# Kernel tuning notes

Hardware: AMD Instinct MI355X
Metric: run time of the kernel (lower is better)

The kernel has to match this reference:

```python
import jax, jax.numpy as jnp
import numpy as np

B, T, V, E, H, NC = 256, 512, 128, 128, 256, 10000


def setup_inputs() -> dict:
    key = jax.random.key(0)
    ks = jax.random.split(key, 10)
    return {
        "dec_input_batch": jax.random.randint(ks[0], (B, T), 0, V),
        "dec_input_lengths": jax.random.randint(ks[1], (B,), 1, T + 1),
        "max_prob_clusters": jax.random.randint(ks[2], (B,), 0, NC),
        "char_embeddings": jax.random.normal(ks[3], (V, E), dtype=jnp.float32) * 0.1,
        "cluster_embeddings": jax.random.normal(ks[4], (NC, H), dtype=jnp.float32) * 0.1,
        "W0": jax.random.normal(ks[5], (E + H + H, 4 * H), dtype=jnp.float32) * 0.05,
        "b0": jnp.zeros((4 * H,), jnp.float32),
        "W1": jax.random.normal(ks[6], (H + H, 4 * H), dtype=jnp.float32) * 0.05,
        "b1": jnp.zeros((4 * H,), jnp.float32),
        "decoderW": jax.random.normal(ks[7], (H, V), dtype=jnp.float32) * (1.0 / (H + V)),
        "decoderB": jnp.zeros((V,), jnp.float32),
    }


def _lstm_step(c, h, x, W, b):
    # TF BasicLSTMCell: gates order i, j, f, o; forget_bias = 1.0
    z = jnp.concatenate([x, h], axis=-1) @ W + b
    i, j, f, o = jnp.split(z, 4, axis=-1)
    c2 = c * jax.nn.sigmoid(f + 1.0) + jax.nn.sigmoid(i) * jnp.tanh(j)
    h2 = jnp.tanh(c2) * jax.nn.sigmoid(o)
    return c2, h2


def reference(dec_input_batch, dec_input_lengths, max_prob_clusters,
              char_embeddings, cluster_embeddings, W0, b0, W1, b1,
              decoderW, decoderB):
    Bb, Tt = dec_input_batch.shape
    Hh = decoderW.shape[0]
    x = char_embeddings[dec_input_batch]                       # [B,T,E]
    clus = cluster_embeddings[max_prob_clusters]               # [B,H]
    clus_bt = jnp.broadcast_to(clus[:, None, :], (Bb, Tt, clus.shape[-1]))
    x = jnp.concatenate([x, clus_bt], axis=-1)                 # [B,T,E+H]
    xs = jnp.transpose(x, (1, 0, 2))                           # [T,B,E+H]
    # dynamic_rnn sequence_length semantics: past length -> zero output, state copied through
    mask = (jnp.arange(Tt)[:, None] < dec_input_lengths[None, :])[..., None]  # [T,B,1]
    zeros = jnp.zeros((Bb, Hh), x.dtype)

    def step(carry, inp):
        c0, h0, c1, h1 = carry
        xt, m = inp
        c0n, h0n = _lstm_step(c0, h0, xt, W0, b0)
        c1n, h1n = _lstm_step(c1, h1, h0n, W1, b1)
        c0 = jnp.where(m, c0n, c0); h0 = jnp.where(m, h0n, h0)
        c1 = jnp.where(m, c1n, c1); h1 = jnp.where(m, h1n, h1)
        out = jnp.where(m, h1n, jnp.zeros_like(h1n))
        return (c0, h0, c1, h1), out

    _, outs = jax.lax.scan(step, (zeros, zeros, zeros, zeros), (xs, mask))
    outs = jnp.transpose(outs, (1, 0, 2))                      # [B,T,H]
    raw_scores = outs @ decoderW + decoderB                    # [B,T,V]
    return raw_scores
```

## Files before the change

kernel.cpp:

```cpp
#include <hip/hip_runtime.h>

#define B_ 256
#define T_ 512
#define V_ 128
#define E_ 128
#define H_ 256
#define FH 1024

#define GROUPS 32
#define RPG 8
#define CWG 16
#define NWG (GROUPS*CWG)

#define HTG 2048
#define GST (GROUPS*HTG)

typedef float f4 __attribute__((ext_vector_type(4)));
typedef unsigned long long ull;

#define OFF_HT0  0
#define OFF_HT1  (OFF_HT0 + 2*GST)
#define OFF_BAR  (OFF_HT1 + 2*GST)
#define BARSZ    (GROUPS*1024)
#define OFF_TP   (OFF_BAR + BARSZ)
#define OFF_CP   (OFF_TP + V_*FH)
#define OFF_WP0  (OFF_CP + B_*FH)
#define OFF_WP1  (OFF_WP0 + CWG*64*64*4)
#define OFF_DWT  (OFF_WP1 + CWG*128*64*4)
#define OFF_B1   (OFF_DWT + V_*H_)
#define OFF_PERM (OFF_B1 + FH)

__device__ __forceinline__ int gcol(int c, int col) {
  int u = col >> 2, g = col & 3;
  return g*256 + c*16 + u;
}

__device__ __forceinline__ float sigm(float x){ return 1.f/(1.f+__expf(-x)); }
__device__ __forceinline__ float tanh_(float x){ return 1.f - 2.f/(1.f+__expf(2.f*x)); }


__global__ void prep_pack(const float* __restrict__ W0, const float* __restrict__ W1,
                          const float* __restrict__ dW, const float* __restrict__ b1,
                          float* __restrict__ ws) {
  float* wp0 = ws + OFF_WP0; float* wp1 = ws + OFF_WP1;
  float* dwT = ws + OFF_DWT; float* b1p = ws + OFF_B1;
  const int N0 = CWG*64*64*4;
  const int N1 = CWG*128*64*4;
  const int N2 = V_*H_;
  const int N3 = FH;
  const int total = N0+N1+N2+N3;
  for (int i = blockIdx.x*blockDim.x + threadIdx.x; i < total; i += gridDim.x*blockDim.x) {
    if (i < N0) {
      int cc = i >> 14; int rem = i & 16383;
      int kb = rem >> 8; int ln = (rem >> 2) & 63; int j = i & 3;
      int k = kb*4 + j;
      wp0[i] = W0[(E_+H_+k)*FH + gcol(cc, ln)];
    } else if (i < N0+N1) {
      int idx = i - N0;
      int cc = idx >> 15; int rem = idx & 32767;
      int kb = rem >> 8; int ln = (rem >> 2) & 63; int j = idx & 3;
      int k2 = kb*4 + j;
      wp1[idx] = W1[k2*FH + gcol(cc, ln)];
    } else if (i < N0+N1+N2) {
      int l = i - N0 - N1;
      int v = l >> 8, k = l & 255;
      dwT[l] = dW[k*V_ + v];
    } else {
      int cc2 = i - N0 - N1 - N2;
      b1p[cc2] = b1[gcol(cc2>>6, cc2&63)];
    }
  }
}

__global__ void prep_tok(const float* __restrict__ cemb, const float* __restrict__ W0,
                         float* __restrict__ ws) {
  __shared__ float ce[E_];
  float* TP = ws + OFF_TP;
  int v = blockIdx.x >> 2, q = blockIdx.x & 3;
  int tid = threadIdx.x;
  if (tid < E_) ce[tid] = cemb[v*E_ + tid];
  __syncthreads();
  int ccol = q*256 + tid;
  int G = gcol(ccol>>6, ccol&63);
  float acc = 0.f;
  for (int e = 0; e < E_; ++e) acc = fmaf(ce[e], W0[e*FH + G], acc);
  TP[v*FH + ccol] = acc;
}

__global__ void prep_clus(const int* __restrict__ clus, const float* __restrict__ clemb,
                          const float* __restrict__ W0, const float* __restrict__ b0,
                          float* __restrict__ ws) {
  __shared__ float ce[H_];
  float* CP = ws + OFF_CP;
  int b = blockIdx.x >> 2, q = blockIdx.x & 3;
  int tid = threadIdx.x;
  int cl = clus[b];
  ce[tid] = clemb[(long long)cl*H_ + tid];
  __syncthreads();
  int ccol = q*256 + tid;
  int G = gcol(ccol>>6, ccol&63);
  float acc = b0[G];
  for (int e = 0; e < H_; ++e) acc = fmaf(ce[e], W0[(E_+e)*FH + G], acc);
  CP[b*FH + ccol] = acc;
}

__global__ void prep_sort(const int* __restrict__ lens, float* __restrict__ ws) {
  __shared__ int sl[B_];
  int* perm = (int*)(ws + OFF_PERM);
  const int i = threadIdx.x;
  sl[i] = lens[i];
  __syncthreads();
  const int li = sl[i];
  int rank = 0;
  for (int j = 0; j < B_; ++j) {
    const int lj = sl[j];
    rank += (lj > li) || (lj == li && j < i);
  }
  perm[rank] = i;
}


__device__ __forceinline__ void st64(float* p, float a, float b) {
  float2 t; t.x = a; t.y = b;
  __hip_atomic_store((ull*)p, __builtin_bit_cast(ull, t),
                     __ATOMIC_RELAXED, __HIP_MEMORY_SCOPE_AGENT);
}

__device__ __forceinline__ void st64_sc0(float* p, float a, float b) {
  float2 t; t.x = a; t.y = b;
  ull v = __builtin_bit_cast(ull, t);
  asm volatile("global_store_dwordx2 %0, %1, off sc0" :: "v"(p), "v"(v) : "memory");
}

__device__ __forceinline__ ull ld64(const void* p) {
  return __hip_atomic_load((const ull*)p, __ATOMIC_RELAXED, __HIP_MEMORY_SCOPE_AGENT);
}

__device__ __forceinline__ unsigned ld32_sc0(const unsigned* p) {
  unsigned v;
  asm volatile("global_load_dword %0, %1, off sc0\n\t"
               "s_waitcnt vmcnt(0)"
               : "=v"(v) : "v"(p) : "memory");
  return v;
}

__device__ __forceinline__ void flag_set(unsigned* p, unsigned v) {
  asm volatile("s_waitcnt vmcnt(0)" ::: "memory");
  __hip_atomic_store(p, v, __ATOMIC_RELAXED, __HIP_MEMORY_SCOPE_AGENT);
}
__device__ __forceinline__ void flag_set_sc0(unsigned* p, unsigned v) {
  asm volatile("s_waitcnt vmcnt(0)" ::: "memory");
  asm volatile("global_store_dword %0, %1, off sc0" :: "v"(p), "v"(v) : "memory");
}

__device__ __forceinline__ void spinAB(const unsigned* fgrp, int lane, unsigned tgt) {
  const unsigned* p = fgrp + (lane & 15)*32 + ((lane >> 5) << 4);
  unsigned v = __hip_atomic_load(p, __ATOMIC_RELAXED, __HIP_MEMORY_SCOPE_AGENT);
  while (!__all((int)(v >= tgt))) {
    __builtin_amdgcn_s_sleep(4);
    v = __hip_atomic_load(p, __ATOMIC_RELAXED, __HIP_MEMORY_SCOPE_AGENT);
  }
}
__device__ __forceinline__ void spinAB_fast(const unsigned* fgrp, int lane, unsigned tgt) {
  const unsigned* p = fgrp + (lane & 15)*32 + ((lane >> 5) << 4);
  unsigned v = ld32_sc0(p);
  int it = 0;
  while (!__all((int)(v >= tgt))) {
    __builtin_amdgcn_s_sleep(2);
    ++it;
    v = (it & 7) ? ld32_sc0(p)
                 : __hip_atomic_load(p, __ATOMIC_RELAXED, __HIP_MEMORY_SCOPE_AGENT);
  }
}

__device__ __forceinline__ void spinB(const unsigned* fgrp, int lane, unsigned tgt) {
  const unsigned* p = fgrp + (lane & 15)*32 + 16;
  unsigned v = __hip_atomic_load(p, __ATOMIC_RELAXED, __HIP_MEMORY_SCOPE_AGENT);
  while (!__all((int)(v >= tgt))) {
    __builtin_amdgcn_s_sleep(4);
    v = __hip_atomic_load(p, __ATOMIC_RELAXED, __HIP_MEMORY_SCOPE_AGENT);
  }
}

__device__ __forceinline__ void lstm_gate(const f4 z, float& cc, float& hh, const bool upd) {
  float ci = sigm(z.x);
  float cj = tanh_(z.y);
  float cf = sigm(z.z + 1.f);
  float co = sigm(z.w);
  float cn = fmaf(cc, cf, ci*cj);
  float hn = tanh_(cn)*co;
  if (upd) { cc = cn; hh = hn; }
}


__global__ __launch_bounds__(256, 2) void lstm_persist(
    const int* __restrict__ toks, const int* __restrict__ lens,
    const float* __restrict__ decB, float* __restrict__ ws, float* __restrict__ out)
{
  const int blk  = blockIdx.x;
  const int xcd  = blk & 7;
  const int j    = blk >> 3;
  const int grp  = (xcd << 2) | ((j & 1) << 1) | (j >> 5);
  const int c    = (j >> 1) & 15;
  const int tid  = threadIdx.x;
  const int lane = tid & 63;
  const int wv   = tid >> 6;
  const int cof  = c*64;

  const int sgrp  = ((grp & 3) << 3) | (grp >> 2);
  const int rbase = sgrp*RPG;
  const int* perm = (const int*)(ws + OFF_PERM);

  float* ht0 = ws + OFF_HT0;
  float* ht1 = ws + OFF_HT1;
  unsigned* fgrp = (unsigned*)(ws + OFF_BAR) + grp*1024;
  const float* TP   = ws + OFF_TP;
  const float* CP   = ws + OFF_CP;
  const float* wp0c = ws + OFF_WP0 + c*(64*64*4);
  const float* wp1c = ws + OFF_WP1 + c*(128*64*4);
  const float* dwT  = ws + OFF_DWT;
  const float* b1p  = ws + OFF_B1;

  __shared__ __align__(16) float h0s[2048];
  __shared__ __align__(16) float h1s[2048];
  __shared__ __align__(16) float za[4][8][64];
  __shared__ __align__(16) float zb[4][8][64];
  __shared__ float ldsW[8][260];
  __shared__ float pred[2][4][64];
  __shared__ unsigned fastSh;

  for (int i = tid; i < 8*H_; i += 256)
    ldsW[i>>8][i&255] = dwT[(c*8 + (i>>8))*H_ + (i&255)];

  unsigned xcc;
  asm volatile("s_getreg_b32 %0, hwreg(HW_REG_XCC_ID)" : "=s"(xcc));
  if (tid == 0)
    __hip_atomic_store(fgrp + 512 + c, xcc + 1u, __ATOMIC_RELAXED, __HIP_MEMORY_SCOPE_AGENT);
  if (wv == 0) {
    const unsigned* p = fgrp + 512 + (lane & 15);
    unsigned v = __hip_atomic_load(p, __ATOMIC_RELAXED, __HIP_MEMORY_SCOPE_AGENT);
    while (!__all((int)(v != 0u))) {
      __builtin_amdgcn_s_sleep(8);
      v = __hip_atomic_load(p, __ATOMIC_RELAXED, __HIP_MEMORY_SCOPE_AGENT);
    }
    const bool same = __all((int)(v == xcc + 1u));
    if (lane == 0) fastSh = same ? 1u : 0u;
  }

  int Lg = lens[perm[rbase + (lane & 7)]];
  Lg = max(Lg, __shfl_xor(Lg, 1));
  Lg = max(Lg, __shfl_xor(Lg, 2));
  Lg = max(Lg, __shfl_xor(Lg, 4));

  const int gu = lane & 15, q = lane >> 4;
  const int rowA = perm[rbase + q], rowB = perm[rbase + q + 4];
  const int lenA = lens[rowA], lenB = lens[rowB];
  const int* tokApt = toks + rowA*T_;
  const int* tokBpt = toks + rowB*T_;
  const f4 cpA = *(const f4*)(CP + rowA*FH + cof + gu*4);
  const f4 cpB = *(const f4*)(CP + rowB*FH + cof + gu*4);
  const f4 b1v = *(const f4*)(b1p + cof + gu*4);
  const int puboff = grp*HTG + (c*16 + gu)*8 + q*2;
  float c0A = 0.f, h0A = 0.f, c0B = 0.f, h0B = 0.f;
  float c1A = 0.f, h1A = 0.f, c1B = 0.f, h1B = 0.f;

  const int pm = lane >> 3, pv = lane & 7;
  const int prm = (pm < 4) ? pm*2 : (pm-4)*2 + 1;
  const int prow = perm[rbase + pm];
  const int plen = lens[prow];
  const float decb = decB[c*8 + pv];
  float* outp = out + (size_t)prow*T_*V_ + c*8 + pv;

  __syncthreads();
  const bool fast = (fastSh != 0u);

  if (wv == 0) {
    f4 zAv = *(const f4*)(TP + tokApt[0]*FH + cof + gu*4) + cpA;
    f4 zBv = *(const f4*)(TP + tokBpt[0]*FH + cof + gu*4) + cpB;
    lstm_gate(zAv, c0A, h0A, 0 < lenA);
    lstm_gate(zBv, c0B, h0B, 0 < lenB);
    if (fast) st64_sc0(ht0 + puboff, h0A, h0B);
    else      st64(ht0 + puboff, h0A, h0B);
    if (lane == 0) {
      if (fast) flag_set_sc0(fgrp + c*32, 1u);
      else      flag_set(fgrp + c*32, 1u);
    }
  } else if (wv == 1) {
    if (lane == 0) {
      if (fast) flag_set_sc0(fgrp + c*32 + 16, 1u);
      else      flag_set(fgrp + c*32 + 16, 1u);
    }
  }

  for (int t = 0; t < Lg; ++t) {
    const int buf = t & 1;

    f4 tpA = {0,0,0,0}, tpB = {0,0,0,0};
    if (wv == 0 && t + 1 < Lg) {
      tpA = *(const f4*)(TP + tokApt[t+1]*FH + cof + gu*4);
      tpB = *(const f4*)(TP + tokBpt[t+1]*FH + cof + gu*4);
    }

    if (fast) spinAB_fast(fgrp, lane, (unsigned)(t + 1));
    else      spinAB(fgrp, lane, (unsigned)(t + 1));
    __atomic_signal_fence(__ATOMIC_SEQ_CST);

    {
      const float* s0 = ht0 + buf*GST + grp*HTG + wv*512 + lane*8;
      const float* s1 = ht1 + buf*GST + grp*HTG + wv*512 + lane*8;
      ull a0, a1, a2, a3, c0, c1, c2, c3;
      if (fast) {
        asm volatile(
          "global_load_dwordx2 %0, %8, off sc0\n\t"
          "global_load_dwordx2 %1, %8, off offset:8 sc0\n\t"
          "global_load_dwordx2 %2, %8, off offset:16 sc0\n\t"
          "global_load_dwordx2 %3, %8, off offset:24 sc0\n\t"
          "global_load_dwordx2 %4, %9, off sc0\n\t"
          "global_load_dwordx2 %5, %9, off offset:8 sc0\n\t"
          "global_load_dwordx2 %6, %9, off offset:16 sc0\n\t"
          "global_load_dwordx2 %7, %9, off offset:24 sc0\n\t"
          "s_waitcnt vmcnt(0)"
          : "=&v"(a0), "=&v"(a1), "=&v"(a2), "=&v"(a3),
            "=&v"(c0), "=&v"(c1), "=&v"(c2), "=&v"(c3)
          : "v"(s0), "v"(s1)
          : "memory");
      } else {
        a0 = ld64(s0);   a1 = ld64(s0+2); a2 = ld64(s0+4); a3 = ld64(s0+6);
        c0 = ld64(s1);   c1 = ld64(s1+2); c2 = ld64(s1+4); c3 = ld64(s1+6);
      }
      float* d0 = h0s + wv*512 + lane*8;
      float* d1 = h1s + wv*512 + lane*8;
      *(ull*)(d0)   = a0; *(ull*)(d0+2) = a1; *(ull*)(d0+4) = a2; *(ull*)(d0+6) = a3;
      *(ull*)(d1)   = c0; *(ull*)(d1+2) = c1; *(ull*)(d1+4) = c2; *(ull*)(d1+6) = c3;
    }

    f4 A0l = {0,0,0,0}, A0h = {0,0,0,0}, A1l = {0,0,0,0}, A1h = {0,0,0,0};
    #pragma unroll 2
    for (int b = 0; b < 16; ++b) {
      const int kb = wv*16 + b;
      const f4 w0 = *(const f4*)(wp0c + kb*256 + lane*4);
      const f4 wl = *(const f4*)(wp1c + kb*256 + lane*4);
      const f4 wu = *(const f4*)(wp1c + (64 + kb)*256 + lane*4);
      #pragma unroll
      for (int jj = 0; jj < 4; ++jj) {
        const int k = kb*4 + jj;
        const float* hb0 = h0s + k*8;
        const float* hb1 = h1s + k*8;
        const f4 h0lo = *(const f4*)(hb0);
        const f4 h0hi = *(const f4*)(hb0 + 4);
        const f4 h1lo = *(const f4*)(hb1);
        const f4 h1hi = *(const f4*)(hb1 + 4);
        const float w0j = w0[jj], wlj = wl[jj], wuj = wu[jj];
        A0l += w0j * h0lo;  A0h += w0j * h0hi;
        A1l += wlj * h0lo + wuj * h1lo;
        A1h += wlj * h0hi + wuj * h1hi;
      }
    }

    float pacc = 0.f;
    {
      const int kq = wv*64;
      #pragma unroll 4
      for (int k2 = 0; k2 < 64; k2 += 4) {
        const f4 w4 = *(const f4*)&ldsW[pv][kq + k2];
        pacc = fmaf(h1s[(kq+k2  )*8 + prm], w4.x, pacc);
        pacc = fmaf(h1s[(kq+k2+1)*8 + prm], w4.y, pacc);
        pacc = fmaf(h1s[(kq+k2+2)*8 + prm], w4.z, pacc);
        pacc = fmaf(h1s[(kq+k2+3)*8 + prm], w4.w, pacc);
      }
    }

    #pragma unroll
    for (int r = 0; r < 4; ++r) {
      za[wv][r][lane]     = A0l[r];
      za[wv][4 + r][lane] = A0h[r];
      zb[wv][r][lane]     = A1l[r];
      zb[wv][4 + r][lane] = A1h[r];
    }
    pred[buf][wv][lane] = pacc;
    __syncthreads();

    if (wv == 0) {
      if (t + 1 < Lg) {
        f4 zA = *(const f4*)&za[0][q*2][gu*4];
        zA += *(const f4*)&za[1][q*2][gu*4];
        zA += *(const f4*)&za[2][q*2][gu*4];
        zA += *(const f4*)&za[3][q*2][gu*4];
        f4 zB = *(const f4*)&za[0][q*2+1][gu*4];
        zB += *(const f4*)&za[1][q*2+1][gu*4];
        zB += *(const f4*)&za[2][q*2+1][gu*4];
        zB += *(const f4*)&za[3][q*2+1][gu*4];
        zA += tpA + cpA;
        zB += tpB + cpB;
        lstm_gate(zA, c0A, h0A, (t+1) < lenA);
        lstm_gate(zB, c0B, h0B, (t+1) < lenB);
        float* pb = ht0 + (buf^1)*GST + puboff;
        if (fast) st64_sc0(pb, h0A, h0B);
        else      st64(pb, h0A, h0B);
        if (lane == 0) {
          if (fast) flag_set_sc0(fgrp + c*32, (unsigned)(t + 2));
          else      flag_set(fgrp + c*32, (unsigned)(t + 2));
        }
      }
    } else if (wv == 1) {
      f4 zA = *(const f4*)&zb[0][q*2][gu*4];
      zA += *(const f4*)&zb[1][q*2][gu*4];
      zA += *(const f4*)&zb[2][q*2][gu*4];
      zA += *(const f4*)&zb[3][q*2][gu*4];
      f4 zB = *(const f4*)&zb[0][q*2+1][gu*4];
      zB += *(const f4*)&zb[1][q*2+1][gu*4];
      zB += *(const f4*)&zb[2][q*2+1][gu*4];
      zB += *(const f4*)&zb[3][q*2+1][gu*4];
      zA += b1v;
      zB += b1v;
      lstm_gate(zA, c1A, h1A, t < lenA);
      lstm_gate(zB, c1B, h1B, t < lenB);
      float* pb = ht1 + (buf^1)*GST + puboff;
      if (fast) st64_sc0(pb, h1A, h1B);
      else      st64(pb, h1A, h1B);
      if (lane == 0) {
        if (fast) flag_set_sc0(fgrp + c*32 + 16, (unsigned)(t + 2));
        else      flag_set(fgrp + c*32 + 16, (unsigned)(t + 2));
      }
    } else if (wv == 2) {
      if (t > 0) {
        float tot = pred[buf][0][lane] + pred[buf][1][lane]
                  + pred[buf][2][lane] + pred[buf][3][lane] + decb;
        if (t - 1 < plen) outp[(size_t)(t-1)*V_] = tot;
      }
    }
  }

  spinB(fgrp, lane, (unsigned)(Lg + 1));
  __atomic_signal_fence(__ATOMIC_SEQ_CST);
  {
    const float* s1 = ht1 + (size_t)(Lg & 1)*GST + grp*HTG + wv*512 + lane*8;
    ull b0 = ld64(s1),   b1 = ld64(s1+2);
    ull b2 = ld64(s1+4), b3 = ld64(s1+6);
    float* d1 = h1s + wv*512 + lane*8;
    *(ull*)(d1)   = b0; *(ull*)(d1+2) = b1;
    *(ull*)(d1+4) = b2; *(ull*)(d1+6) = b3;
  }
  {
    float pacc = 0.f;
    const int kq = wv*64;
    #pragma unroll 4
    for (int k2 = 0; k2 < 64; k2 += 4) {
      const f4 w4 = *(const f4*)&ldsW[pv][kq + k2];
      pacc = fmaf(h1s[(kq+k2  )*8 + prm], w4.x, pacc);
      pacc = fmaf(h1s[(kq+k2+1)*8 + prm], w4.y, pacc);
      pacc = fmaf(h1s[(kq+k2+2)*8 + prm], w4.z, pacc);
      pacc = fmaf(h1s[(kq+k2+3)*8 + prm], w4.w, pacc);
    }
    pred[Lg & 1][wv][lane] = pacc;
  }
  __syncthreads();
  if (wv == 2) {
    float tot = pred[Lg & 1][0][lane] + pred[Lg & 1][1][lane]
              + pred[Lg & 1][2][lane] + pred[Lg & 1][3][lane] + decb;
    if (Lg - 1 < plen) outp[(size_t)(Lg-1)*V_] = tot;
  }
}


extern "C" void kernel_launch(void* const* d_in, const int* in_sizes, int n_in,
                              void* d_out, int out_size, void* d_ws, size_t ws_size,
                              hipStream_t stream) {
  const int*   toks  = (const int*)d_in[0];
  const int*   lens  = (const int*)d_in[1];
  const int*   clus  = (const int*)d_in[2];
  const float* cemb  = (const float*)d_in[3];
  const float* clemb = (const float*)d_in[4];
  const float* W0    = (const float*)d_in[5];
  const float* b0    = (const float*)d_in[6];
  const float* W1    = (const float*)d_in[7];
  const float* b1    = (const float*)d_in[8];
  const float* dW    = (const float*)d_in[9];
  const float* decB  = (const float*)d_in[10];
  float* out = (float*)d_out;
  float* ws  = (float*)d_ws;

  hipMemsetAsync(out, 0, (size_t)B_*T_*V_*sizeof(float), stream);
  hipMemsetAsync(ws, 0, (size_t)(OFF_BAR + BARSZ)*sizeof(float), stream);

  prep_pack<<<1024, 256, 0, stream>>>(W0, W1, dW, b1, ws);
  prep_tok <<<V_*4, 256, 0, stream>>>(cemb, W0, ws);
  prep_clus<<<B_*4, 256, 0, stream>>>(clus, clemb, W0, b0, ws);
  prep_sort<<<1, 256, 0, stream>>>(lens, ws);
  lstm_persist<<<NWG, 256, 0, stream>>>(toks, lens, decB, ws, out);
}
```

Baseline: 4.574 ms.

## Merge two column chunks per 512-thread workgroup in persistent LSTM kernel

The persistent kernel now runs 256 workgroups of 512 threads instead of 512 workgroups of 256. Each workgroup handles two 64-column gate chunks, one per four-wave half, and both halves share the staged h0/h1 buffers and the reduction arrays in LDS. The aim is to cut redundant global hidden-state loads and the number of workgroups polling the flags. The decoder weight tile is no longer staged in LDS and is read directly from global memory each step, which may add per-step load latency. Both halves also write the same LDS h buffers redundantly.

```diff
diff --git a/kernel.cpp b/kernel.cpp
--- a/kernel.cpp
+++ b/kernel.cpp
@@ -10,7 +10,8 @@
 #define GROUPS 32
 #define RPG 8
 #define CWG 16
-#define NWG (GROUPS*CWG)
+#define WGPG 8
+#define NWG (GROUPS*WGPG)
 
 #define HTG 2048
 #define GST (GROUPS*HTG)
@@ -193,21 +194,25 @@
 }
 
 
-__global__ __launch_bounds__(256, 2) void lstm_persist(
+__global__ __launch_bounds__(512, 2) void lstm_persist(
     const int* __restrict__ toks, const int* __restrict__ lens,
     const float* __restrict__ decB, float* __restrict__ ws, float* __restrict__ out)
 {
   const int blk  = blockIdx.x;
   const int xcd  = blk & 7;
   const int j    = blk >> 3;
-  const int grp  = (xcd << 2) | ((j & 1) << 1) | (j >> 5);
-  const int c    = (j >> 1) & 15;
+  const int cc   = j & 7;
+  const int loc  = j >> 3;
+  const int grp  = (xcd << 2) | loc;
   const int tid  = threadIdx.x;
   const int lane = tid & 63;
   const int wv   = tid >> 6;
-  const int cof  = c*64;
-
-  const int sgrp  = ((grp & 3) << 3) | (grp >> 2);
+  const int ch   = wv >> 2;
+  const int kwin = wv & 3;
+  const int ca   = cc*2 + ch;
+  const int cof  = ca*64;
+
+  const int sgrp  = (loc << 3) | xcd;
   const int rbase = sgrp*RPG;
   const int* perm = (const int*)(ws + OFF_PERM);
 
@@ -216,28 +221,24 @@
   unsigned* fgrp = (unsigned*)(ws + OFF_BAR) + grp*1024;
   const float* TP   = ws + OFF_TP;
   const float* CP   = ws + OFF_CP;
-  const float* wp0c = ws + OFF_WP0 + c*(64*64*4);
-  const float* wp1c = ws + OFF_WP1 + c*(128*64*4);
+  const float* wp0c = ws + OFF_WP0 + ca*(64*64*4);
+  const float* wp1c = ws + OFF_WP1 + ca*(128*64*4);
   const float* dwT  = ws + OFF_DWT;
   const float* b1p  = ws + OFF_B1;
 
-  __shared__ __align__(16) float h0s[2048];
-  __shared__ __align__(16) float h1s[2048];
-  __shared__ __align__(16) float za[4][8][64];
-  __shared__ __align__(16) float zb[4][8][64];
-  __shared__ float ldsW[8][260];
-  __shared__ float pred[2][4][64];
+  __shared__ __align__(16) float h0s[4*512];
+  __shared__ __align__(16) float h1s[4*512];
+  __shared__ __align__(16) float za[4][8][128];
+  __shared__ __align__(16) float zb[4][8][128];
+  __shared__ float pred[2][4][2][64];
   __shared__ unsigned fastSh;
-
-  for (int i = tid; i < 8*H_; i += 256)
-    ldsW[i>>8][i&255] = dwT[(c*8 + (i>>8))*H_ + (i&255)];
 
   unsigned xcc;
   asm volatile("s_getreg_b32 %0, hwreg(HW_REG_XCC_ID)" : "=s"(xcc));
   if (tid == 0)
-    __hip_atomic_store(fgrp + 512 + c, xcc + 1u, __ATOMIC_RELAXED, __HIP_MEMORY_SCOPE_AGENT);
+    __hip_atomic_store(fgrp + 512 + cc, xcc + 1u, __ATOMIC_RELAXED, __HIP_MEMORY_SCOPE_AGENT);
   if (wv == 0) {
-    const unsigned* p = fgrp + 512 + (lane & 15);
+    const unsigned* p = fgrp + 512 + (lane & 7);
     unsigned v = __hip_atomic_load(p, __ATOMIC_RELAXED, __HIP_MEMORY_SCOPE_AGENT);
     while (!__all((int)(v != 0u))) {
       __builtin_amdgcn_s_sleep(8);
@@ -260,7 +261,7 @@
   const f4 cpA = *(const f4*)(CP + rowA*FH + cof + gu*4);
   const f4 cpB = *(const f4*)(CP + rowB*FH + cof + gu*4);
   const f4 b1v = *(const f4*)(b1p + cof + gu*4);
-  const int puboff = grp*HTG + (c*16 + gu)*8 + q*2;
+  const int puboff = grp*HTG + (ca*16 + gu)*8 + q*2;
   float c0A = 0.f, h0A = 0.f, c0B = 0.f, h0B = 0.f;
   float c1A = 0.f, h1A = 0.f, c1B = 0.f, h1B = 0.f;
 
@@ -268,13 +269,14 @@
   const int prm = (pm < 4) ? pm*2 : (pm-4)*2 + 1;
   const int prow = perm[rbase + pm];
   const int plen = lens[prow];
-  const float decb = decB[c*8 + pv];
-  float* outp = out + (size_t)prow*T_*V_ + c*8 + pv;
+  const float decb = decB[ca*8 + pv];
+  float* outp = out + (size_t)prow*T_*V_ + ca*8 + pv;
+  const float* dwRow = dwT + (ca*8 + pv)*H_;
 
   __syncthreads();
   const bool fast = (fastSh != 0u);
 
-  if (wv == 0) {
+  if ((wv & 3) == 0) {
     f4 zAv = *(const f4*)(TP + tokApt[0]*FH + cof + gu*4) + cpA;
     f4 zBv = *(const f4*)(TP + tokBpt[0]*FH + cof + gu*4) + cpB;
     lstm_gate(zAv, c0A, h0A, 0 < lenA);
@@ -282,13 +284,13 @@
     if (fast) st64_sc0(ht0 + puboff, h0A, h0B);
     else      st64(ht0 + puboff, h0A, h0B);
     if (lane == 0) {
-      if (fast) flag_set_sc0(fgrp + c*32, 1u);
-      else      flag_set(fgrp + c*32, 1u);
-    }
-  } else if (wv == 1) {
+      if (fast) flag_set_sc0(fgrp + ca*32, 1u);
+      else      flag_set(fgrp + ca*32, 1u);
+    }
+  } else if ((wv & 3) == 1) {
     if (lane == 0) {
-      if (fast) flag_set_sc0(fgrp + c*32 + 16, 1u);
-      else      flag_set(fgrp + c*32 + 16, 1u);
+      if (fast) flag_set_sc0(fgrp + ca*32 + 16, 1u);
+      else      flag_set(fgrp + ca*32 + 16, 1u);
     }
   }
 
@@ -296,7 +298,7 @@
     const int buf = t & 1;
 
     f4 tpA = {0,0,0,0}, tpB = {0,0,0,0};
-    if (wv == 0 && t + 1 < Lg) {
+    if ((wv & 3) == 0 && t + 1 < Lg) {
       tpA = *(const f4*)(TP + tokApt[t+1]*FH + cof + gu*4);
       tpB = *(const f4*)(TP + tokBpt[t+1]*FH + cof + gu*4);
     }
@@ -306,8 +308,8 @@
     __atomic_signal_fence(__ATOMIC_SEQ_CST);
 
     {
-      const float* s0 = ht0 + buf*GST + grp*HTG + wv*512 + lane*8;
-      const float* s1 = ht1 + buf*GST + grp*HTG + wv*512 + lane*8;
+      const float* s0 = ht0 + buf*GST + grp*HTG + kwin*512 + lane*8;
+      const float* s1 = ht1 + buf*GST + grp*HTG + kwin*512 + lane*8;
       ull a0, a1, a2, a3, c0, c1, c2, c3;
       if (fast) {
         asm volatile(
@@ -328,8 +330,8 @@
         a0 = ld64(s0);   a1 = ld64(s0+2); a2 = ld64(s0+4); a3 = ld64(s0+6);
         c0 = ld64(s1);   c1 = ld64(s1+2); c2 = ld64(s1+4); c3 = ld64(s1+6);
       }
-      float* d0 = h0s + wv*512 + lane*8;
-      float* d1 = h1s + wv*512 + lane*8;
+      float* d0 = h0s + kwin*512 + lane*8;
+      float* d1 = h1s + kwin*512 + lane*8;
       *(ull*)(d0)   = a0; *(ull*)(d0+2) = a1; *(ull*)(d0+4) = a2; *(ull*)(d0+6) = a3;
       *(ull*)(d1)   = c0; *(ull*)(d1+2) = c1; *(ull*)(d1+4) = c2; *(ull*)(d1+6) = c3;
     }
@@ -337,15 +339,15 @@
     f4 A0l = {0,0,0,0}, A0h = {0,0,0,0}, A1l = {0,0,0,0}, A1h = {0,0,0,0};
     #pragma unroll 2
     for (int b = 0; b < 16; ++b) {
-      const int kb = wv*16 + b;
+      const int kb = kwin*16 + b;
       const f4 w0 = *(const f4*)(wp0c + kb*256 + lane*4);
       const f4 wl = *(const f4*)(wp1c + kb*256 + lane*4);
       const f4 wu = *(const f4*)(wp1c + (64 + kb)*256 + lane*4);
       #pragma unroll
       for (int jj = 0; jj < 4; ++jj) {
-        const int k = kb*4 + jj;
-        const float* hb0 = h0s + k*8;
-        const float* hb1 = h1s + k*8;
+        const int kl = b*4 + jj;
+        const float* hb0 = h0s + kwin*512 + kl*8;
+        const float* hb1 = h1s + kwin*512 + kl*8;
         const f4 h0lo = *(const f4*)(hb0);
         const f4 h0hi = *(const f4*)(hb0 + 4);
         const f4 h1lo = *(const f4*)(hb1);
@@ -359,37 +361,38 @@
 
     float pacc = 0.f;
     {
-      const int kq = wv*64;
+      const float* wrow = dwRow + kwin*64;
       #pragma unroll 4
       for (int k2 = 0; k2 < 64; k2 += 4) {
-        const f4 w4 = *(const f4*)&ldsW[pv][kq + k2];
-        pacc = fmaf(h1s[(kq+k2  )*8 + prm], w4.x, pacc);
-        pacc = fmaf(h1s[(kq+k2+1)*8 + prm], w4.y, pacc);
-        pacc = fmaf(h1s[(kq+k2+2)*8 + prm], w4.z, pacc);
-        pacc = fmaf(h1s[(kq+k2+3)*8 + prm], w4.w, pacc);
+        const f4 w4 = *(const f4*)(wrow + k2);
+        pacc = fmaf(h1s[kwin*512 + (k2  )*8 + prm], w4.x, pacc);
+        pacc = fmaf(h1s[kwin*512 + (k2+1)*8 + prm], w4.y, pacc);
+        pacc = fmaf(h1s[kwin*512 + (k2+2)*8 + prm], w4.z, pacc);
+        pacc = fmaf(h1s[kwin*512 + (k2+3)*8 + prm], w4.w, pacc);
       }
     }
 
     #pragma unroll
     for (int r = 0; r < 4; ++r) {
-      za[wv][r][lane]     = A0l[r];
-      za[wv][4 + r][lane] = A0h[r];
-      zb[wv][r][lane]     = A1l[r];
-      zb[wv][4 + r][lane] = A1h[r];
-    }
-    pred[buf][wv][lane] = pacc;
+      za[kwin][r][ch*64 + lane]     = A0l[r];
+      za[kwin][4 + r][ch*64 + lane] = A0h[r];
+      zb[kwin][r][ch*64 + lane]     = A1l[r];
+      zb[kwin][4 + r][ch*64 + lane] = A1h[r];
+    }
+    pred[buf][kwin][ch][lane] = pacc;
     __syncthreads();
 
-    if (wv == 0) {
+    const int cb = ch*64;
+    if ((wv & 3) == 0) {
       if (t + 1 < Lg) {
-        f4 zA = *(const f4*)&za[0][q*2][gu*4];
-        zA += *(const f4*)&za[1][q*2][gu*4];
-        zA += *(const f4*)&za[2][q*2][gu*4];
-        zA += *(const f4*)&za[3][q*2][gu*4];
-        f4 zB = *(const f4*)&za[0][q*2+1][gu*4];
-        zB += *(const f4*)&za[1][q*2+1][gu*4];
-        zB += *(const f4*)&za[2][q*2+1][gu*4];
-        zB += *(const f4*)&za[3][q*2+1][gu*4];
+        f4 zA = *(const f4*)&za[0][q*2][cb + gu*4];
+        zA += *(const f4*)&za[1][q*2][cb + gu*4];
+        zA += *(const f4*)&za[2][q*2][cb + gu*4];
+        zA += *(const f4*)&za[3][q*2][cb + gu*4];
+        f4 zB = *(const f4*)&za[0][q*2+1][cb + gu*4];
+        zB += *(const f4*)&za[1][q*2+1][cb + gu*4];
+        zB += *(const f4*)&za[2][q*2+1][cb + gu*4];
+        zB += *(const f4*)&za[3][q*2+1][cb + gu*4];
         zA += tpA + cpA;
         zB += tpB + cpB;
         lstm_gate(zA, c0A, h0A, (t+1) < lenA);
@@ -398,19 +401,19 @@
         if (fast) st64_sc0(pb, h0A, h0B);
         else      st64(pb, h0A, h0B);
         if (lane == 0) {
-          if (fast) flag_set_sc0(fgrp + c*32, (unsigned)(t + 2));
-          else      flag_set(fgrp + c*32, (unsigned)(t + 2));
+          if (fast) flag_set_sc0(fgrp + ca*32, (unsigned)(t + 2));
+          else      flag_set(fgrp + ca*32, (unsigned)(t + 2));
         }
       }
-    } else if (wv == 1) {
-      f4 zA = *(const f4*)&zb[0][q*2][gu*4];
-      zA += *(const f4*)&zb[1][q*2][gu*4];
-      zA += *(const f4*)&zb[2][q*2][gu*4];
-      zA += *(const f4*)&zb[3][q*2][gu*4];
-      f4 zB = *(const f4*)&zb[0][q*2+1][gu*4];
-      zB += *(const f4*)&zb[1][q*2+1][gu*4];
-      zB += *(const f4*)&zb[2][q*2+1][gu*4];
-      zB += *(const f4*)&zb[3][q*2+1][gu*4];
+    } else if ((wv & 3) == 1) {
+      f4 zA = *(const f4*)&zb[0][q*2][cb + gu*4];
+      zA += *(const f4*)&zb[1][q*2][cb + gu*4];
+      zA += *(const f4*)&zb[2][q*2][cb + gu*4];
+      zA += *(const f4*)&zb[3][q*2][cb + gu*4];
+      f4 zB = *(const f4*)&zb[0][q*2+1][cb + gu*4];
+      zB += *(const f4*)&zb[1][q*2+1][cb + gu*4];
+      zB += *(const f4*)&zb[2][q*2+1][cb + gu*4];
+      zB += *(const f4*)&zb[3][q*2+1][cb + gu*4];
       zA += b1v;
       zB += b1v;
       lstm_gate(zA, c1A, h1A, t < lenA);
@@ -419,13 +422,13 @@
       if (fast) st64_sc0(pb, h1A, h1B);
       else      st64(pb, h1A, h1B);
       if (lane == 0) {
-        if (fast) flag_set_sc0(fgrp + c*32 + 16, (unsigned)(t + 2));
-        else      flag_set(fgrp + c*32 + 16, (unsigned)(t + 2));
-      }
-    } else if (wv == 2) {
+        if (fast) flag_set_sc0(fgrp + ca*32 + 16, (unsigned)(t + 2));
+        else      flag_set(fgrp + ca*32 + 16, (unsigned)(t + 2));
+      }
+    } else if ((wv & 3) == 2) {
       if (t > 0) {
-        float tot = pred[buf][0][lane] + pred[buf][1][lane]
-                  + pred[buf][2][lane] + pred[buf][3][lane] + decb;
+        float tot = pred[buf][0][ch][lane] + pred[buf][1][ch][lane]
+                  + pred[buf][2][ch][lane] + pred[buf][3][ch][lane] + decb;
         if (t - 1 < plen) outp[(size_t)(t-1)*V_] = tot;
       }
     }
@@ -434,30 +437,30 @@
   spinB(fgrp, lane, (unsigned)(Lg + 1));
   __atomic_signal_fence(__ATOMIC_SEQ_CST);
   {
-    const float* s1 = ht1 + (size_t)(Lg & 1)*GST + grp*HTG + wv*512 + lane*8;
+    const float* s1 = ht1 + (size_t)(Lg & 1)*GST + grp*HTG + kwin*512 + lane*8;
     ull b0 = ld64(s1),   b1 = ld64(s1+2);
     ull b2 = ld64(s1+4), b3 = ld64(s1+6);
-    float* d1 = h1s + wv*512 + lane*8;
+    float* d1 = h1s + kwin*512 + lane*8;
     *(ull*)(d1)   = b0; *(ull*)(d1+2) = b1;
     *(ull*)(d1+4) = b2; *(ull*)(d1+6) = b3;
   }
   {
     float pacc = 0.f;
-    const int kq = wv*64;
+    const float* wrow = dwRow + kwin*64;
     #pragma unroll 4
     for (int k2 = 0; k2 < 64; k2 += 4) {
-      const f4 w4 = *(const f4*)&ldsW[pv][kq + k2];
-      pacc = fmaf(h1s[(kq+k2  )*8 + prm], w4.x, pacc);
-      pacc = fmaf(h1s[(kq+k2+1)*8 + prm], w4.y, pacc);
-      pacc = fmaf(h1s[(kq+k2+2)*8 + prm], w4.z, pacc);
-      pacc = fmaf(h1s[(kq+k2+3)*8 + prm], w4.w, pacc);
-    }
-    pred[Lg & 1][wv][lane] = pacc;
+      const f4 w4 = *(const f4*)(wrow + k2);
+      pacc = fmaf(h1s[kwin*512 + (k2  )*8 + prm], w4.x, pacc);
+      pacc = fmaf(h1s[kwin*512 + (k2+1)*8 + prm], w4.y, pacc);
+      pacc = fmaf(h1s[kwin*512 + (k2+2)*8 + prm], w4.z, pacc);
+      pacc = fmaf(h1s[kwin*512 + (k2+3)*8 + prm], w4.w, pacc);
+    }
+    pred[Lg & 1][kwin][ch][lane] = pacc;
   }
   __syncthreads();
-  if (wv == 2) {
-    float tot = pred[Lg & 1][0][lane] + pred[Lg & 1][1][lane]
-              + pred[Lg & 1][2][lane] + pred[Lg & 1][3][lane] + decb;
+  if ((wv & 3) == 2) {
+    float tot = pred[Lg & 1][0][ch][lane] + pred[Lg & 1][1][ch][lane]
+              + pred[Lg & 1][2][ch][lane] + pred[Lg & 1][3][ch][lane] + decb;
     if (Lg - 1 < plen) outp[(size_t)(Lg-1)*V_] = tot;
   }
 }
@@ -487,5 +490,5 @@
   prep_tok <<<V_*4, 256, 0, stream>>>(cemb, W0, ws);
   prep_clus<<<B_*4, 256, 0, stream>>>(clus, clemb, W0, b0, ws);
   prep_sort<<<1, 256, 0, stream>>>(lens, ws);
-  lstm_persist<<<NWG, 256, 0, stream>>>(toks, lens, decB, ws, out);
-}
+  lstm_persist<<<NWG, 512, 0, stream>>>(toks, lens, decB, ws, out);
+}
```

After: 6.311 ms. 38.0% more time.

## Split layer-0 and layer-1 phases to publish h0 before waiting on h1

Applied to the files above, without the earlier changes.

Each step used to wait for both layer-0 and layer-1 hidden-state flags, then do both matvecs before publishing either result. Now each workgroup waits only for layer-0 flags, computes the layer-0 gates, and publishes h0 for the next step using an LDS counter in place of a full barrier. Only after that does it wait for the layer-1 flags and do the layer-1 work. This shortens the cross-workgroup critical path of the recurrence, but adds a second spin-wait per step and LDS atomic polling.

```diff
diff --git a/kernel.cpp b/kernel.cpp
--- a/kernel.cpp
+++ b/kernel.cpp
@@ -153,16 +153,16 @@
   asm volatile("global_store_dword %0, %1, off sc0" :: "v"(p), "v"(v) : "memory");
 }
 
-__device__ __forceinline__ void spinAB(const unsigned* fgrp, int lane, unsigned tgt) {
-  const unsigned* p = fgrp + (lane & 15)*32 + ((lane >> 5) << 4);
+__device__ __forceinline__ void spinA(const unsigned* fgrp, int lane, unsigned tgt) {
+  const unsigned* p = fgrp + (lane & 15)*32;
   unsigned v = __hip_atomic_load(p, __ATOMIC_RELAXED, __HIP_MEMORY_SCOPE_AGENT);
   while (!__all((int)(v >= tgt))) {
     __builtin_amdgcn_s_sleep(4);
     v = __hip_atomic_load(p, __ATOMIC_RELAXED, __HIP_MEMORY_SCOPE_AGENT);
   }
 }
-__device__ __forceinline__ void spinAB_fast(const unsigned* fgrp, int lane, unsigned tgt) {
-  const unsigned* p = fgrp + (lane & 15)*32 + ((lane >> 5) << 4);
+__device__ __forceinline__ void spinA_fast(const unsigned* fgrp, int lane, unsigned tgt) {
+  const unsigned* p = fgrp + (lane & 15)*32;
   unsigned v = ld32_sc0(p);
   int it = 0;
   while (!__all((int)(v >= tgt))) {
@@ -172,13 +172,23 @@
                  : __hip_atomic_load(p, __ATOMIC_RELAXED, __HIP_MEMORY_SCOPE_AGENT);
   }
 }
-
 __device__ __forceinline__ void spinB(const unsigned* fgrp, int lane, unsigned tgt) {
   const unsigned* p = fgrp + (lane & 15)*32 + 16;
   unsigned v = __hip_atomic_load(p, __ATOMIC_RELAXED, __HIP_MEMORY_SCOPE_AGENT);
   while (!__all((int)(v >= tgt))) {
     __builtin_amdgcn_s_sleep(4);
     v = __hip_atomic_load(p, __ATOMIC_RELAXED, __HIP_MEMORY_SCOPE_AGENT);
+  }
+}
+__device__ __forceinline__ void spinB_fast(const unsigned* fgrp, int lane, unsigned tgt) {
+  const unsigned* p = fgrp + (lane & 15)*32 + 16;
+  unsigned v = ld32_sc0(p);
+  int it = 0;
+  while (!__all((int)(v >= tgt))) {
+    __builtin_amdgcn_s_sleep(2);
+    ++it;
+    v = (it & 7) ? ld32_sc0(p)
+                 : __hip_atomic_load(p, __ATOMIC_RELAXED, __HIP_MEMORY_SCOPE_AGENT);
   }
 }
 
@@ -228,6 +238,9 @@
   __shared__ float ldsW[8][260];
   __shared__ float pred[2][4][64];
   __shared__ unsigned fastSh;
+  __shared__ unsigned zaCtr;
+
+  if (tid == 0) zaCtr = 0u;
 
   for (int i = tid; i < 8*H_; i += 256)
     ldsW[i>>8][i&255] = dwT[(c*8 + (i>>8))*H_ + (i&255)];
@@ -301,59 +314,117 @@
       tpB = *(const f4*)(TP + tokBpt[t+1]*FH + cof + gu*4);
     }
 
-    if (fast) spinAB_fast(fgrp, lane, (unsigned)(t + 1));
-    else      spinAB(fgrp, lane, (unsigned)(t + 1));
+    if (fast) spinA_fast(fgrp, lane, (unsigned)(t + 1));
+    else      spinA(fgrp, lane, (unsigned)(t + 1));
     __atomic_signal_fence(__ATOMIC_SEQ_CST);
 
     {
       const float* s0 = ht0 + buf*GST + grp*HTG + wv*512 + lane*8;
-      const float* s1 = ht1 + buf*GST + grp*HTG + wv*512 + lane*8;
-      ull a0, a1, a2, a3, c0, c1, c2, c3;
+      ull a0, a1, a2, a3;
       if (fast) {
         asm volatile(
-          "global_load_dwordx2 %0, %8, off sc0\n\t"
-          "global_load_dwordx2 %1, %8, off offset:8 sc0\n\t"
-          "global_load_dwordx2 %2, %8, off offset:16 sc0\n\t"
-          "global_load_dwordx2 %3, %8, off offset:24 sc0\n\t"
-          "global_load_dwordx2 %4, %9, off sc0\n\t"
-          "global_load_dwordx2 %5, %9, off offset:8 sc0\n\t"
-          "global_load_dwordx2 %6, %9, off offset:16 sc0\n\t"
-          "global_load_dwordx2 %7, %9, off offset:24 sc0\n\t"
+          "global_load_dwordx2 %0, %4, off sc0\n\t"
+          "global_load_dwordx2 %1, %4, off offset:8 sc0\n\t"
+          "global_load_dwordx2 %2, %4, off offset:16 sc0\n\t"
+          "global_load_dwordx2 %3, %4, off offset:24 sc0\n\t"
           "s_waitcnt vmcnt(0)"
-          : "=&v"(a0), "=&v"(a1), "=&v"(a2), "=&v"(a3),
-            "=&v"(c0), "=&v"(c1), "=&v"(c2), "=&v"(c3)
-          : "v"(s0), "v"(s1)
+          : "=&v"(a0), "=&v"(a1), "=&v"(a2), "=&v"(a3)
+          : "v"(s0)
           : "memory");
       } else {
-        a0 = ld64(s0);   a1 = ld64(s0+2); a2 = ld64(s0+4); a3 = ld64(s0+6);
-        c0 = ld64(s1);   c1 = ld64(s1+2); c2 = ld64(s1+4); c3 = ld64(s1+6);
+        a0 = ld64(s0); a1 = ld64(s0+2); a2 = ld64(s0+4); a3 = ld64(s0+6);
       }
       float* d0 = h0s + wv*512 + lane*8;
+      *(ull*)(d0)   = a0; *(ull*)(d0+2) = a1; *(ull*)(d0+4) = a2; *(ull*)(d0+6) = a3;
+    }
+
+    f4 A0l = {0,0,0,0}, A0h = {0,0,0,0};
+    #pragma unroll 4
+    for (int b = 0; b < 16; ++b) {
+      const int kb = wv*16 + b;
+      const f4 w0 = *(const f4*)(wp0c + kb*256 + lane*4);
+      #pragma unroll
+      for (int jj = 0; jj < 4; ++jj) {
+        const int k = kb*4 + jj;
+        const f4 h0lo = *(const f4*)(h0s + k*8);
+        const f4 h0hi = *(const f4*)(h0s + k*8 + 4);
+        A0l += w0[jj] * h0lo;
+        A0h += w0[jj] * h0hi;
+      }
+    }
+    #pragma unroll
+    for (int r = 0; r < 4; ++r) {
+      za[wv][r][lane]     = A0l[r];
+      za[wv][4 + r][lane] = A0h[r];
+    }
+    if (lane == 0)
+      __hip_atomic_fetch_add(&zaCtr, 1u, __ATOMIC_ACQ_REL, __HIP_MEMORY_SCOPE_WORKGROUP);
+
+    if (wv == 0 && t + 1 < Lg) {
+      while (__hip_atomic_load(&zaCtr, __ATOMIC_ACQUIRE, __HIP_MEMORY_SCOPE_WORKGROUP)
+             < 4u*(unsigned)(t + 1))
+        __builtin_amdgcn_s_sleep(1);
+      __atomic_signal_fence(__ATOMIC_SEQ_CST);
+      f4 zA = *(const f4*)&za[0][q*2][gu*4];
+      zA += *(const f4*)&za[1][q*2][gu*4];
+      zA += *(const f4*)&za[2][q*2][gu*4];
+      zA += *(const f4*)&za[3][q*2][gu*4];
+      f4 zB = *(const f4*)&za[0][q*2+1][gu*4];
+      zB += *(const f4*)&za[1][q*2+1][gu*4];
+      zB += *(const f4*)&za[2][q*2+1][gu*4];
+      zB += *(const f4*)&za[3][q*2+1][gu*4];
+      zA += tpA + cpA;
+      zB += tpB + cpB;
+      lstm_gate(zA, c0A, h0A, (t+1) < lenA);
+      lstm_gate(zB, c0B, h0B, (t+1) < lenB);
+      float* pb = ht0 + (buf^1)*GST + puboff;
+      if (fast) st64_sc0(pb, h0A, h0B);
+      else      st64(pb, h0A, h0B);
+      if (lane == 0) {
+        if (fast) flag_set_sc0(fgrp + c*32, (unsigned)(t + 2));
+        else      flag_set(fgrp + c*32, (unsigned)(t + 2));
+      }
+    }
+
+    if (fast) spinB_fast(fgrp, lane, (unsigned)(t + 1));
+    else      spinB(fgrp, lane, (unsigned)(t + 1));
+    __atomic_signal_fence(__ATOMIC_SEQ_CST);
+
+    {
+      const float* s1 = ht1 + buf*GST + grp*HTG + wv*512 + lane*8;
+      ull c0, c1, c2, c3;
+      if (fast) {
+        asm volatile(
+          "global_load_dwordx2 %0, %4, off sc0\n\t"
+          "global_load_dwordx2 %1, %4, off offset:8 sc0\n\t"
+          "global_load_dwordx2 %2, %4, off offset:16 sc0\n\t"
+          "global_load_dwordx2 %3, %4, off offset:24 sc0\n\t"
+          "s_waitcnt vmcnt(0)"
+          : "=&v"(c0), "=&v"(c1), "=&v"(c2), "=&v"(c3)
+          : "v"(s1)
+          : "memory");
+      } else {
+        c0 = ld64(s1); c1 = ld64(s1+2); c2 = ld64(s1+4); c3 = ld64(s1+6);
+      }
       float* d1 = h1s + wv*512 + lane*8;
-      *(ull*)(d0)   = a0; *(ull*)(d0+2) = a1; *(ull*)(d0+4) = a2; *(ull*)(d0+6) = a3;
       *(ull*)(d1)   = c0; *(ull*)(d1+2) = c1; *(ull*)(d1+4) = c2; *(ull*)(d1+6) = c3;
     }
 
-    f4 A0l = {0,0,0,0}, A0h = {0,0,0,0}, A1l = {0,0,0,0}, A1h = {0,0,0,0};
+    f4 A1l = {0,0,0,0}, A1h = {0,0,0,0};
     #pragma unroll 2
     for (int b = 0; b < 16; ++b) {
       const int kb = wv*16 + b;
-      const f4 w0 = *(const f4*)(wp0c + kb*256 + lane*4);
       const f4 wl = *(const f4*)(wp1c + kb*256 + lane*4);
       const f4 wu = *(const f4*)(wp1c + (64 + kb)*256 + lane*4);
       #pragma unroll
       for (int jj = 0; jj < 4; ++jj) {
         const int k = kb*4 + jj;
-        const float* hb0 = h0s + k*8;
-        const float* hb1 = h1s + k*8;
-        const f4 h0lo = *(const f4*)(hb0);
-        const f4 h0hi = *(const f4*)(hb0 + 4);
-        const f4 h1lo = *(const f4*)(hb1);
-        const f4 h1hi = *(const f4*)(hb1 + 4);
-        const float w0j = w0[jj], wlj = wl[jj], wuj = wu[jj];
-        A0l += w0j * h0lo;  A0h += w0j * h0hi;
-        A1l += wlj * h0lo + wuj * h1lo;
-        A1h += wlj * h0hi + wuj * h1hi;
+        const f4 h0lo = *(const f4*)(h0s + k*8);
+        const f4 h0hi = *(const f4*)(h0s + k*8 + 4);
+        const f4 h1lo = *(const f4*)(h1s + k*8);
+        const f4 h1hi = *(const f4*)(h1s + k*8 + 4);
+        A1l += wl[jj] * h0lo + wu[jj] * h1lo;
+        A1h += wl[jj] * h0hi + wu[jj] * h1hi;
       }
     }
 
@@ -372,37 +443,13 @@
 
     #pragma unroll
     for (int r = 0; r < 4; ++r) {
-      za[wv][r][lane]     = A0l[r];
-      za[wv][4 + r][lane] = A0h[r];
       zb[wv][r][lane]     = A1l[r];
       zb[wv][4 + r][lane] = A1h[r];
     }
     pred[buf][wv][lane] = pacc;
     __syncthreads();
 
-    if (wv == 0) {
-      if (t + 1 < Lg) {
-        f4 zA = *(const f4*)&za[0][q*2][gu*4];
-        zA += *(const f4*)&za[1][q*2][gu*4];
-        zA += *(const f4*)&za[2][q*2][gu*4];
-        zA += *(const f4*)&za[3][q*2][gu*4];
-        f4 zB = *(const f4*)&za[0][q*2+1][gu*4];
-        zB += *(const f4*)&za[1][q*2+1][gu*4];
-        zB += *(const f4*)&za[2][q*2+1][gu*4];
-        zB += *(const f4*)&za[3][q*2+1][gu*4];
-        zA += tpA + cpA;
-        zB += tpB + cpB;
-        lstm_gate(zA, c0A, h0A, (t+1) < lenA);
-        lstm_gate(zB, c0B, h0B, (t+1) < lenB);
-        float* pb = ht0 + (buf^1)*GST + puboff;
-        if (fast) st64_sc0(pb, h0A, h0B);
-        else      st64(pb, h0A, h0B);
-        if (lane == 0) {
-          if (fast) flag_set_sc0(fgrp + c*32, (unsigned)(t + 2));
-          else      flag_set(fgrp + c*32, (unsigned)(t + 2));
-        }
-      }
-    } else if (wv == 1) {
+    if (wv == 1) {
       f4 zA = *(const f4*)&zb[0][q*2][gu*4];
       zA += *(const f4*)&zb[1][q*2][gu*4];
       zA += *(const f4*)&zb[2][q*2][gu*4];
```

Measured after the change: 5.995 ms. 31.1% more time.
